# Kernel optimization log

Hardware: AMD Instinct MI355X
Metric: run time of the kernel (lower is better)

The kernel has to match this reference:

```python
import jax, jax.numpy as jnp
import numpy as np


def setup_inputs() -> dict:
    key = jax.random.key(0)
    ks = jax.random.split(key, 4)
    B, L, D, H, C = 32, 512, 768, 100, 45
    sequence_output = jax.random.normal(ks[0], (B, L, D), dtype=jnp.float32)
    valid_ids = jax.random.randint(ks[1], (B, L), 0, 2, dtype=jnp.int32)
    W1 = jax.random.normal(ks[2], (H, D), dtype=jnp.float32) * 0.02
    b1 = jnp.zeros((H,), jnp.float32)
    W2 = jax.random.normal(ks[3], (C, H), dtype=jnp.float32) * 0.02
    b2 = jnp.zeros((C,), jnp.float32)
    return {"sequence_output": sequence_output, "valid_ids": valid_ids,
            "W1": W1, "b1": b1, "W2": W2, "b2": b2}


def reference(sequence_output, valid_ids, W1, b1, W2, b2):
    # Vectorized equivalent of the nested compaction loop:
    # for each row i, valid tokens (valid_ids==1) are packed to the front,
    # remaining slots stay zero.
    B, L, D = sequence_output.shape
    valid = valid_ids == 1                      # [B, L] bool
    pos = jnp.cumsum(valid, axis=1) - 1         # destination index for valid tokens
    pos = jnp.where(valid, pos, L)              # invalid tokens -> dump slot L
    bidx = jnp.arange(B)[:, None]               # [B, 1]
    buf = jnp.zeros((B, L + 1, D), sequence_output.dtype)
    buf = buf.at[bidx, pos].set(sequence_output)  # scatter rows in parallel
    valid_output = buf[:, :L]                   # drop the dump slot
    # Dropout (p=0.3, training) in the original is stochastic; omitted here
    # (identity / eval mode) so the baseline is deterministic.
    h = valid_output @ W1.T + b1                # [B, L, 100]
    logits = h @ W2.T + b2                      # [B, L, num_labels]
    return logits.reshape(-1, W2.shape[0])      # [B*L, num_labels]
```

## Files before the change

### kernel.cpp

```cpp
#include <hip/hip_runtime.h>
#include <hip/hip_bf16.h>
#include <stdint.h>

#define Bb 32
#define Ll 512
#define Dd 768
#define Hh 100
#define Cc 45
#define CP 48
#define MROWS (Bb * Ll)

typedef __attribute__((ext_vector_type(8))) short short8;
typedef __attribute__((ext_vector_type(4))) float f32x4;

__device__ __forceinline__ unsigned short f2bf_rne(float v) {
    uint32_t u = __float_as_uint(v);
    return (unsigned short)((u + 0x7fffu + ((u >> 16) & 1u)) >> 16);
}

__global__ void prep_wc(const float* __restrict__ W1, const float* __restrict__ b1,
                        const float* __restrict__ W2, const float* __restrict__ b2,
                        unsigned short* __restrict__ Wc, float* __restrict__ bc) {
    const int c     = blockIdx.x / 3;
    const int chunk = blockIdx.x % 3;
    const int t     = threadIdx.x;
    const int d     = chunk * 256 + t;
    if (c >= Cc) {
        Wc[c * Dd + d] = 0;
    } else {
        float a = 0.f;
        const float* w1p = W1 + d;
        const float* w2p = W2 + c * Hh;
        #pragma unroll 4
        for (int h = 0; h < Hh; ++h) a += w2p[h] * w1p[h * Dd];
        Wc[c * Dd + d] = f2bf_rne(a);
    }
    if (blockIdx.x == 0 && t < CP) {
        float s = (t < Cc) ? b2[t] : 0.f;
        if (t < Cc)
            for (int h = 0; h < Hh; ++h) s += W2[t * Hh + h] * b1[h];
        bc[t] = s;
    }
}

__global__ __launch_bounds__(256, 4) void gemm_out(
    const float* __restrict__ x,
    const int* __restrict__ valid,
    const unsigned short* __restrict__ Wc,
    const float* __restrict__ bc,
    float* __restrict__ out)
{
    __shared__ int   g[Ll];
    __shared__ int   wsum[4];
    __shared__ float red[4][12][64];

    const int t    = threadIdx.x;
    const int wave = t >> 6;
    const int lane = t & 63;
    const int quad = lane >> 4;
    const int nn   = lane & 15;

    const int rowbase = blockIdx.x * 16;
    const int b       = rowbase >> 9;
    const int p0      = rowbase & (Ll - 1);

    g[t] = -1; g[t + 256] = -1;
    int2 vv = ((const int2*)(valid + b * Ll))[t];
    int v0 = (vv.x == 1), v1 = (vv.y == 1);
    int ps = v0 + v1;
    __syncthreads();
    int incl = ps;
    #pragma unroll
    for (int d = 1; d < 64; d <<= 1) {
        int n = __shfl_up(incl, d, 64);
        if (lane >= d) incl += n;
    }
    if (lane == 63) wsum[wave] = incl;
    __syncthreads();
    int woff = 0;
    #pragma unroll
    for (int w = 0; w < 4; ++w) woff += (w < wave) ? wsum[w] : 0;
    int e = woff + incl - ps;
    if (v0) g[e] = 2 * t;
    if (v1) g[e + v0] = 2 * t + 1;
    __syncthreads();

    const int srcl = g[p0 + nn];
    const int src  = (srcl >= 0) ? (b * Ll + srcl) : -1;
    const float* xp = x + (long)(src >= 0 ? src : 0) * Dd + wave * 192 + quad * 8;
    const unsigned short* bp = Wc + nn * Dd + wave * 192 + quad * 8;

    f32x4 acc0 = {0.f, 0.f, 0.f, 0.f};
    f32x4 acc1 = {0.f, 0.f, 0.f, 0.f};
    f32x4 acc2 = {0.f, 0.f, 0.f, 0.f};

    #pragma unroll
    for (int ks = 0; ks < 6; ++ks) {
        union { short8 s; uint32_t u[4]; } A;
        A.u[0] = 0; A.u[1] = 0; A.u[2] = 0; A.u[3] = 0;
        if (src >= 0) {
            f32x4 xa = *(const f32x4*)(xp + ks * 32);
            f32x4 xb = *(const f32x4*)(xp + ks * 32 + 4);
            A.u[0] = (__float_as_uint(xa.x) >> 16) | (__float_as_uint(xa.y) & 0xffff0000u);
            A.u[1] = (__float_as_uint(xa.z) >> 16) | (__float_as_uint(xa.w) & 0xffff0000u);
            A.u[2] = (__float_as_uint(xb.x) >> 16) | (__float_as_uint(xb.y) & 0xffff0000u);
            A.u[3] = (__float_as_uint(xb.z) >> 16) | (__float_as_uint(xb.w) & 0xffff0000u);
        }
        short8 b0 = *(const short8*)(bp + 0 * 16 * Dd + ks * 32);
        short8 b1v = *(const short8*)(bp + 1 * 16 * Dd + ks * 32);
        short8 b2v = *(const short8*)(bp + 2 * 16 * Dd + ks * 32);
        acc0 = __builtin_amdgcn_mfma_f32_16x16x32_bf16(A.s, b0,  acc0, 0, 0, 0);
        acc1 = __builtin_amdgcn_mfma_f32_16x16x32_bf16(A.s, b1v, acc1, 0, 0, 0);
        acc2 = __builtin_amdgcn_mfma_f32_16x16x32_bf16(A.s, b2v, acc2, 0, 0, 0);
    }

    #pragma unroll
    for (int r = 0; r < 4; ++r) {
        red[wave][0 * 4 + r][lane] = acc0[r];
        red[wave][1 * 4 + r][lane] = acc1[r];
        red[wave][2 * 4 + r][lane] = acc2[r];
    }
    __syncthreads();

    #pragma unroll
    for (int oo = 0; oo < 3; ++oo) {
        int o = t + oo * 256;
        int j = o >> 6, l = o & 63;
        float s = red[0][j][l] + red[1][j][l] + red[2][j][l] + red[3][j][l];
        int q = l >> 4, n2 = l & 15;
        int ct = j >> 2, r = j & 3;
        int col = ct * 16 + n2;
        if (col < Cc) {
            int row = rowbase + q * 4 + r;
            out[row * Cc + col] = s + bc[col];
        }
    }
}

extern "C" void kernel_launch(void* const* d_in, const int* in_sizes, int n_in,
                              void* d_out, int out_size, void* d_ws, size_t ws_size,
                              hipStream_t stream) {
    const float* seq   = (const float*)d_in[0];
    const int*   valid = (const int*)d_in[1];
    const float* W1    = (const float*)d_in[2];
    const float* b1    = (const float*)d_in[3];
    const float* W2    = (const float*)d_in[4];
    const float* b2    = (const float*)d_in[5];
    float* out = (float*)d_out;

    unsigned short* Wc = (unsigned short*)d_ws;
    float* bc          = (float*)((char*)d_ws + 73728);

    prep_wc<<<CP * 3, 256, 0, stream>>>(W1, b1, W2, b2, Wc, bc);
    gemm_out<<<MROWS / 16, 256, 0, stream>>>(seq, valid, Wc, bc, out);
}
```

Before: 113.7 us.

## Precompute compaction gather indices once per batch row in prep kernel

The prefix-sum compaction of valid_ids moves out of the GEMM kernel into the prep kernel. It is computed once per batch row and written to a global gather array, so each of the 1024 GEMM blocks no longer redoes the 512-element scan and its block barriers. The fused-weight computation is also reorganised into 512-thread blocks with four independent accumulators. The trade-off is an extra global index read per GEMM block and a dependency on the prep kernel's output.

Measured after the change: 105.2 us. 7.5% less time.

```diff
diff --git a/kernel.cpp b/kernel.cpp
--- a/kernel.cpp
+++ b/kernel.cpp
@@ -9,6 +9,7 @@
 #define Cc 45
 #define CP 48
 #define MROWS (Bb * Ll)
+#define WC_BLOCKS 72
 
 typedef __attribute__((ext_vector_type(8))) short short8;
 typedef __attribute__((ext_vector_type(4))) float f32x4;
@@ -18,40 +19,73 @@
     return (unsigned short)((u + 0x7fffu + ((u >> 16) & 1u)) >> 16);
 }
 
-__global__ void prep_wc(const float* __restrict__ W1, const float* __restrict__ b1,
-                        const float* __restrict__ W2, const float* __restrict__ b2,
-                        unsigned short* __restrict__ Wc, float* __restrict__ bc) {
-    const int c     = blockIdx.x / 3;
-    const int chunk = blockIdx.x % 3;
-    const int t     = threadIdx.x;
-    const int d     = chunk * 256 + t;
-    if (c >= Cc) {
-        Wc[c * Dd + d] = 0;
-    } else {
-        float a = 0.f;
-        const float* w1p = W1 + d;
-        const float* w2p = W2 + c * Hh;
-        #pragma unroll 4
-        for (int h = 0; h < Hh; ++h) a += w2p[h] * w1p[h * Dd];
-        Wc[c * Dd + d] = f2bf_rne(a);
+__global__ __launch_bounds__(512) void prep(
+    const float* __restrict__ W1, const float* __restrict__ b1,
+    const float* __restrict__ W2, const float* __restrict__ b2,
+    const int* __restrict__ valid,
+    unsigned short* __restrict__ Wc, float* __restrict__ bc,
+    int* __restrict__ gather)
+{
+    const int t = threadIdx.x;
+
+    if (blockIdx.x < WC_BLOCKS) {
+        const int o = blockIdx.x * 512 + t;
+        const int c = o / Dd;
+        const int d = o - c * Dd;
+        if (c >= Cc) { Wc[o] = 0; return; }
+        const float* w1 = W1 + d;
+        const float* w2 = W2 + c * Hh;
+        float a0 = 0.f, a1 = 0.f, a2 = 0.f, a3 = 0.f;
+        #pragma unroll
+        for (int h = 0; h < Hh; h += 4) {
+            a0 += w2[h + 0] * w1[(h + 0) * Dd];
+            a1 += w2[h + 1] * w1[(h + 1) * Dd];
+            a2 += w2[h + 2] * w1[(h + 2) * Dd];
+            a3 += w2[h + 3] * w1[(h + 3) * Dd];
+        }
+        Wc[o] = f2bf_rne((a0 + a1) + (a2 + a3));
+        return;
     }
-    if (blockIdx.x == 0 && t < CP) {
-        float s = (t < Cc) ? b2[t] : 0.f;
-        if (t < Cc)
+
+    if (blockIdx.x < WC_BLOCKS + Bb) {
+        const int b    = blockIdx.x - WC_BLOCKS;
+        const int wave = t >> 6;
+        const int lane = t & 63;
+        __shared__ int wsum[8];
+        int v = (valid[b * Ll + t] == 1) ? 1 : 0;
+        gather[b * Ll + t] = -1;
+        int incl = v;
+        #pragma unroll
+        for (int d = 1; d < 64; d <<= 1) {
+            int n = __shfl_up(incl, d, 64);
+            if (lane >= d) incl += n;
+        }
+        if (lane == 63) wsum[wave] = incl;
+        __syncthreads();
+        int woff = 0;
+        #pragma unroll
+        for (int w = 0; w < 8; ++w) woff += (w < wave) ? wsum[w] : 0;
+        if (v) gather[b * Ll + woff + incl - 1] = t;
+        return;
+    }
+
+    if (t < CP) {
+        float s = 0.f;
+        if (t < Cc) {
+            s = b2[t];
             for (int h = 0; h < Hh; ++h) s += W2[t * Hh + h] * b1[h];
+        }
         bc[t] = s;
     }
 }
 
 __global__ __launch_bounds__(256, 4) void gemm_out(
     const float* __restrict__ x,
-    const int* __restrict__ valid,
     const unsigned short* __restrict__ Wc,
     const float* __restrict__ bc,
+    const int* __restrict__ gather,
     float* __restrict__ out)
 {
-    __shared__ int   g[Ll];
-    __shared__ int   wsum[4];
     __shared__ float red[4][12][64];
 
     const int t    = threadIdx.x;
@@ -64,28 +98,7 @@
     const int b       = rowbase >> 9;
     const int p0      = rowbase & (Ll - 1);
 
-    g[t] = -1; g[t + 256] = -1;
-    int2 vv = ((const int2*)(valid + b * Ll))[t];
-    int v0 = (vv.x == 1), v1 = (vv.y == 1);
-    int ps = v0 + v1;
-    __syncthreads();
-    int incl = ps;
-    #pragma unroll
-    for (int d = 1; d < 64; d <<= 1) {
-        int n = __shfl_up(incl, d, 64);
-        if (lane >= d) incl += n;
-    }
-    if (lane == 63) wsum[wave] = incl;
-    __syncthreads();
-    int woff = 0;
-    #pragma unroll
-    for (int w = 0; w < 4; ++w) woff += (w < wave) ? wsum[w] : 0;
-    int e = woff + incl - ps;
-    if (v0) g[e] = 2 * t;
-    if (v1) g[e + v0] = 2 * t + 1;
-    __syncthreads();
-
-    const int srcl = g[p0 + nn];
+    const int srcl = gather[rowbase + nn];
     const int src  = (srcl >= 0) ? (b * Ll + srcl) : -1;
     const float* xp = x + (long)(src >= 0 ? src : 0) * Dd + wave * 192 + quad * 8;
     const unsigned short* bp = Wc + nn * Dd + wave * 192 + quad * 8;
@@ -106,7 +119,7 @@
             A.u[2] = (__float_as_uint(xb.x) >> 16) | (__float_as_uint(xb.y) & 0xffff0000u);
             A.u[3] = (__float_as_uint(xb.z) >> 16) | (__float_as_uint(xb.w) & 0xffff0000u);
         }
-        short8 b0 = *(const short8*)(bp + 0 * 16 * Dd + ks * 32);
+        short8 b0  = *(const short8*)(bp + 0 * 16 * Dd + ks * 32);
         short8 b1v = *(const short8*)(bp + 1 * 16 * Dd + ks * 32);
         short8 b2v = *(const short8*)(bp + 2 * 16 * Dd + ks * 32);
         acc0 = __builtin_amdgcn_mfma_f32_16x16x32_bf16(A.s, b0,  acc0, 0, 0, 0);
@@ -150,7 +163,8 @@
 
     unsigned short* Wc = (unsigned short*)d_ws;
     float* bc          = (float*)((char*)d_ws + 73728);
+    int* gather        = (int*)((char*)d_ws + 73728 + 256);
 
-    prep_wc<<<CP * 3, 256, 0, stream>>>(W1, b1, W2, b2, Wc, bc);
-    gemm_out<<<MROWS / 16, 256, 0, stream>>>(seq, valid, Wc, bc, out);
+    prep<<<WC_BLOCKS + Bb + 1, 512, 0, stream>>>(W1, b1, W2, b2, valid, Wc, bc, gather);
+    gemm_out<<<MROWS / 16, 256, 0, stream>>>(seq, Wc, bc, gather, out);
 }
```
